# Optimization experiments

Measured on AMD Instinct MI355X. Metric: run time of the kernel, lower is better.

Reference implementation:

```python
import jax, jax.numpy as jnp
import numpy as np

N = 4096
D_MODEL = 512


def setup_inputs() -> dict:
    key = jax.random.key(0)
    ks = jax.random.split(key, 5)
    scale = 1.0 / np.sqrt(D_MODEL)
    return {
        "x": jax.random.normal(ks[0], (N, D_MODEL), dtype=jnp.float32),
        "Wq": jax.random.normal(ks[1], (D_MODEL, D_MODEL), dtype=jnp.float32) * scale,
        "Wk": jax.random.normal(ks[2], (D_MODEL, D_MODEL), dtype=jnp.float32) * scale,
        "Wv": jax.random.normal(ks[3], (D_MODEL, D_MODEL), dtype=jnp.float32) * scale,
        "Ws": jax.random.normal(ks[4], (1, D_MODEL), dtype=jnp.float32) * scale,
    }


def reference(x, Wq, Wk, Wv, Ws):
    # x: [N, d]; torch nn.Linear(bias=False) computes x @ W.T
    Q = x @ Wq.T  # [N, d]
    K = x @ Wk.T  # [N, d]
    V = x @ Wv.T  # [N, d]
    sigma = jnp.clip(x @ Ws.T, 0.001, 1.0)  # [N, 1]

    # prior association: Gaussian kernel over |i - j| with per-row sigma
    pos = jnp.arange(sigma.shape[0], dtype=jnp.float32)
    diff = jnp.abs(pos[:, None] - pos[None, :])  # [N, N]
    gaussian = jnp.exp(-0.5 * (diff / sigma) ** 2) / jnp.sqrt(2.0 * jnp.pi * sigma)
    P = gaussian / (gaussian.sum(axis=1, keepdims=True) + 1e-8)

    scale = jnp.sqrt(jnp.float32(x.shape[-1]))
    S = jax.nn.softmax((Q @ K.T) / scale, axis=-1)  # [N, N]
    Z = S @ V  # [N, d]
    return Z, P, S
```

## Files before the change

kernel.cpp:

```cpp
#include <hip/hip_runtime.h>
#include <math.h>

#define N_TOK 4096
#define DM 512

typedef _Float16 f16x8 __attribute__((ext_vector_type(8)));
typedef _Float16 f16x4 __attribute__((ext_vector_type(4)));
typedef float f32x4 __attribute__((ext_vector_type(4)));

__device__ __forceinline__ void async_ld16(const ushort* g, ushort* l) {
  __builtin_amdgcn_global_load_lds(
      (const __attribute__((address_space(1))) void*)g,
      (__attribute__((address_space(3))) void*)l, 16, 0, 0);
}

template <int N>
__device__ __forceinline__ void vm_wait() {
  asm volatile("s_waitcnt vmcnt(%0)" ::"i"(N) : "memory");
}

__global__ __launch_bounds__(256) void pack_sigma(
    const float* __restrict__ x, const float* __restrict__ Wq,
    const float* __restrict__ Wk, const float* __restrict__ Wv,
    const float* __restrict__ Ws, _Float16* __restrict__ x16,
    _Float16* __restrict__ Wc16, float* __restrict__ sg) {
  const int b = blockIdx.x;
  const int t = threadIdx.x;
  if (b < 2048) {
    int i = b * 1024 + t * 4;
    float4 v = *(const float4*)&x[i];
    f16x4 o;
    o.x = (_Float16)v.x; o.y = (_Float16)v.y;
    o.z = (_Float16)v.z; o.w = (_Float16)v.w;
    *(f16x4*)&x16[i] = o;
    int col = (t * 4) & 511;
    float4 w = *(const float4*)&Ws[col];
    float p = v.x * w.x + v.y * w.y + v.z * w.z + v.w * w.w;
    __shared__ float red[256];
    red[t] = p;
    __syncthreads();
    int lt = t & 127;
    for (int off = 64; off > 0; off >>= 1) {
      if (lt < off) red[t] += red[t + off];
      __syncthreads();
    }
    if (lt == 0) {
      float s = red[t];
      sg[2 * b + (t >> 7)] = fminf(fmaxf(s, 0.001f), 1.0f);
    }
  } else {
    int e = (b - 2048) * 1024 + t * 4;
    const float* src;
    int le = e & (DM * DM - 1);
    if (e < DM * DM) src = Wq + le;
    else if (e < 2 * DM * DM) src = Wk + le;
    else src = Wv + le;
    float4 v = *(const float4*)src;
    f16x4 o;
    o.x = (_Float16)v.x; o.y = (_Float16)v.y;
    o.z = (_Float16)v.z; o.w = (_Float16)v.w;
    *(f16x4*)&Wc16[e] = o;
  }
}

template <int BM, int BN, int BK, int NT, int EPI, int FUSE_P>
__global__ __launch_bounds__(256) void gemm_pipe(
    const _Float16* __restrict__ A, int lda, const _Float16* __restrict__ B,
    int ldb, float scale, float* __restrict__ Cf, _Float16* __restrict__ D0,
    _Float16* __restrict__ D1, _Float16* __restrict__ D2,
    const float* __restrict__ sigma, float* __restrict__ P) {
  constexpr int TB = (BM + BN) * BK;
  constexpr int ACH = BM * BK / 8;
  constexpr int BCH = BN * BK / 8;
  constexpr int L = (ACH + BCH) / 256;
  constexpr int MI = BM / 32;
  constexpr int NJ = BN / 32;
  __shared__ _Float16 lds[3 * TB];
  const int t = threadIdx.x;

  if (FUSE_P && blockIdx.y >= 64) {
    float* red = (float*)lds;
    const int pidx = (blockIdx.y - 64) * 4 + blockIdx.x;
    const int w = t >> 6, lane = t & 63;
#pragma unroll 1
    for (int rr = 0; rr < 4; ++rr) {
      const int i = pidx * 4 + rr;
      const float sgv = sigma[i];
      const float inv2 = -0.5f / (sgv * sgv);
      const float cc = rsqrtf(6.283185307179586f * sgv);
      float4 g[4];
      float sum = 0.f;
#pragma unroll
      for (int r = 0; r < 4; ++r) {
        int j = r * 1024 + t * 4;
        float d0 = (float)(i - j);
        float d1 = d0 - 1.f, d2 = d0 - 2.f, d3 = d0 - 3.f;
        g[r].x = __expf(inv2 * d0 * d0) * cc;
        g[r].y = __expf(inv2 * d1 * d1) * cc;
        g[r].z = __expf(inv2 * d2 * d2) * cc;
        g[r].w = __expf(inv2 * d3 * d3) * cc;
        sum += g[r].x + g[r].y + g[r].z + g[r].w;
      }
#pragma unroll
      for (int off = 32; off > 0; off >>= 1) sum += __shfl_xor(sum, off);
      if (lane == 0) red[w] = sum;
      __syncthreads();
      const float inv = 1.0f / (red[0] + red[1] + red[2] + red[3] + 1e-8f);
      float* Prow = P + (size_t)i * N_TOK;
#pragma unroll
      for (int r = 0; r < 4; ++r) {
        g[r].x *= inv; g[r].y *= inv; g[r].z *= inv; g[r].w *= inv;
        *(float4*)&Prow[r * 1024 + t * 4] = g[r];
      }
      __syncthreads();
    }
    return;
  }

  const int w = t >> 6, Ln = t & 63;
  const int wm = (w >> 1) * (BM / 2), wn = (w & 1) * (BN / 2);
  const int row = Ln & 15, quad = Ln >> 4;
  const int bm = blockIdx.y * BM, bn = blockIdx.x * BN;

  f32x4 acc[MI][NJ] = {{}};

  const ushort* gp[L];
#pragma unroll
  for (int k = 0; k < L; ++k) {
    int c = t + k * 256;
    if (c < ACH) {
      int r = c / (BK / 8), c8 = c % (BK / 8);
      gp[k] = (const ushort*)(A + (size_t)(bm + r) * lda + c8 * 8);
    } else {
      int cb = c - ACH;
      int r = cb / (BK / 8), c8 = cb % (BK / 8);
      gp[k] = (const ushort*)(B + (size_t)(bn + r) * ldb + c8 * 8);
    }
  }

  auto stage = [&](int buf) {
    _Float16* dst = lds + buf * TB;
#pragma unroll
    for (int k = 0; k < L; ++k) {
      async_ld16(gp[k], (ushort*)(dst + (t + k * 256) * 8));
      gp[k] += BK;
    }
  };

  stage(0);
  stage(1);

  for (int tt = 0; tt < NT; ++tt) {
    const int cur = tt % 3;
    if (tt + 2 < NT) stage((tt + 2) % 3);
    if (tt < NT - 2) vm_wait<2 * L>();
    else if (tt == NT - 2) vm_wait<L>();
    else vm_wait<0>();
    __builtin_amdgcn_s_barrier();

    const _Float16* Ah = lds + cur * TB;
    const _Float16* Bh = Ah + BM * BK;
    f16x8 af[BK / 32][MI], bf[BK / 32][NJ];
#pragma unroll
    for (int kk = 0; kk < BK / 32; ++kk) {
#pragma unroll
      for (int i = 0; i < MI; ++i)
        af[kk][i] =
            *(const f16x8*)&Ah[(wm + i * 16 + row) * BK + kk * 32 + quad * 8];
#pragma unroll
      for (int j = 0; j < NJ; ++j)
        bf[kk][j] =
            *(const f16x8*)&Bh[(wn + j * 16 + row) * BK + kk * 32 + quad * 8];
    }
#pragma unroll
    for (int kk = 0; kk < BK / 32; ++kk)
#pragma unroll
      for (int i = 0; i < MI; ++i)
#pragma unroll
        for (int j = 0; j < NJ; ++j)
          acc[i][j] = __builtin_amdgcn_mfma_f32_16x16x32_f16(
              af[kk][i], bf[kk][j], acc[i][j], 0, 0, 0);

    asm volatile("s_waitcnt lgkmcnt(0)" ::: "memory");
    __builtin_amdgcn_s_barrier();
  }

  if constexpr (EPI == 1) {
    const int region = bn >> 9;
    _Float16* D = (region == 0) ? D0 : ((region == 1) ? D1 : D2);
#pragma unroll
    for (int i = 0; i < MI; ++i)
#pragma unroll
      for (int j = 0; j < NJ; ++j)
#pragma unroll
        for (int r = 0; r < 4; ++r) {
          int gr = bm + wm + i * 16 + quad * 4 + r;
          int nn = (bn & 511) + wn + j * 16 + row;
          D[(size_t)gr * 512 + nn] = (_Float16)acc[i][j][r];
        }
  } else if constexpr (EPI == 3) {
#pragma unroll
    for (int i = 0; i < MI; ++i)
#pragma unroll
      for (int j = 0; j < NJ; ++j)
#pragma unroll
        for (int r = 0; r < 4; ++r) {
          int gr = bm + wm + i * 16 + quad * 4 + r;
          int gc = bn + wn + j * 16 + row;
          D0[(size_t)gr * N_TOK + gc] = (_Float16)(acc[i][j][r] * scale);
        }
  } else {
#pragma unroll
    for (int i = 0; i < MI; ++i)
#pragma unroll
      for (int j = 0; j < NJ; ++j)
#pragma unroll
        for (int r = 0; r < 4; ++r) {
          int gr = bm + wm + i * 16 + quad * 4 + r;
          int gc = bn + wn + j * 16 + row;
          Cf[(size_t)gr * DM + gc] = acc[i][j][r];
        }
  }
}

__global__ __launch_bounds__(256) void transpose16(
    const _Float16* __restrict__ V16, _Float16* __restrict__ VT) {
  __shared__ _Float16 T[32][34];
  const int t = threadIdx.x;
  const int r = t >> 3, c4 = (t & 7) * 4;
  f16x4 v = *(const f16x4*)&V16[(size_t)(blockIdx.y * 32 + r) * 512 +
                                blockIdx.x * 32 + c4];
  T[r][c4] = v.x; T[r][c4 + 1] = v.y; T[r][c4 + 2] = v.z; T[r][c4 + 3] = v.w;
  __syncthreads();
  f16x4 o;
  o.x = T[c4][r]; o.y = T[c4 + 1][r]; o.z = T[c4 + 2][r]; o.w = T[c4 + 3][r];
  *(f16x4*)&VT[(size_t)(blockIdx.x * 32 + r) * 4096 + blockIdx.y * 32 + c4] = o;
}

__global__ __launch_bounds__(256) void softmax_kernel(
    _Float16* __restrict__ Sc, float* __restrict__ S) {
  __shared__ float red[256];
  const int t = threadIdx.x;
  _Float16* Srow16 = Sc + (size_t)blockIdx.x * N_TOK;
  float* Srow = S + (size_t)blockIdx.x * N_TOK;
  float f[16];
  float m = -INFINITY;
#pragma unroll
  for (int r = 0; r < 4; ++r) {
    f16x4 h = *(const f16x4*)&Srow16[r * 1024 + t * 4];
    f[r * 4 + 0] = (float)h.x; f[r * 4 + 1] = (float)h.y;
    f[r * 4 + 2] = (float)h.z; f[r * 4 + 3] = (float)h.w;
    m = fmaxf(m, fmaxf(fmaxf(f[r * 4], f[r * 4 + 1]),
                       fmaxf(f[r * 4 + 2], f[r * 4 + 3])));
  }
  red[t] = m;
  __syncthreads();
  for (int off = 128; off > 0; off >>= 1) {
    if (t < off) red[t] = fmaxf(red[t], red[t + off]);
    __syncthreads();
  }
  m = red[0];
  __syncthreads();
  float sum = 0.f;
#pragma unroll
  for (int i = 0; i < 16; ++i) {
    f[i] = __expf(f[i] - m);
    sum += f[i];
  }
  red[t] = sum;
  __syncthreads();
  for (int off = 128; off > 0; off >>= 1) {
    if (t < off) red[t] += red[t + off];
    __syncthreads();
  }
  const float inv = 1.0f / red[0];
#pragma unroll
  for (int r = 0; r < 4; ++r) {
    float4 o;
    o.x = f[r * 4 + 0] * inv; o.y = f[r * 4 + 1] * inv;
    o.z = f[r * 4 + 2] * inv; o.w = f[r * 4 + 3] * inv;
    *(float4*)&Srow[r * 1024 + t * 4] = o;
    f16x4 h;
    h.x = (_Float16)o.x; h.y = (_Float16)o.y;
    h.z = (_Float16)o.z; h.w = (_Float16)o.w;
    *(f16x4*)&Srow16[r * 1024 + t * 4] = h;
  }
}

__global__ __launch_bounds__(256) void tailP(const float* __restrict__ sigma,
                                             float* __restrict__ P) {
  __shared__ float red[256];
  const int t = threadIdx.x;
  const int i = blockIdx.x;
  const float sg = sigma[i];
  const float inv2 = -0.5f / (sg * sg);
  const float c = rsqrtf(6.283185307179586f * sg);
  float4 g[4];
  float sum = 0.f;
#pragma unroll
  for (int r = 0; r < 4; ++r) {
    int j = r * 1024 + t * 4;
    float d0 = (float)(i - j);
    float d1 = d0 - 1.f, d2 = d0 - 2.f, d3 = d0 - 3.f;
    g[r].x = __expf(inv2 * d0 * d0) * c;
    g[r].y = __expf(inv2 * d1 * d1) * c;
    g[r].z = __expf(inv2 * d2 * d2) * c;
    g[r].w = __expf(inv2 * d3 * d3) * c;
    sum += g[r].x + g[r].y + g[r].z + g[r].w;
  }
  red[t] = sum;
  __syncthreads();
  for (int off = 128; off > 0; off >>= 1) {
    if (t < off) red[t] += red[t + off];
    __syncthreads();
  }
  const float inv = 1.0f / (red[0] + 1e-8f);
  float* Prow = P + (size_t)i * N_TOK;
#pragma unroll
  for (int r = 0; r < 4; ++r) {
    g[r].x *= inv; g[r].y *= inv; g[r].z *= inv; g[r].w *= inv;
    *(float4*)&Prow[r * 1024 + t * 4] = g[r];
  }
}

extern "C" void kernel_launch(void* const* d_in, const int* in_sizes, int n_in,
                              void* d_out, int out_size, void* d_ws,
                              size_t ws_size, hipStream_t stream) {
  const float* x = (const float*)d_in[0];
  const float* Wq = (const float*)d_in[1];
  const float* Wk = (const float*)d_in[2];
  const float* Wv = (const float*)d_in[3];
  const float* Ws = (const float*)d_in[4];

  float* out = (float*)d_out;
  float* Z = out;
  float* Pout = Z + (size_t)N_TOK * DM;
  float* S = Pout + (size_t)N_TOK * N_TOK;

  const size_t E = (size_t)N_TOK * DM;

  _Float16* x16 = (_Float16*)d_ws;
  _Float16* Wc16 = x16 + E;
  float* sg = (float*)(Wc16 + 3 * DM * DM);
  _Float16* stage = (_Float16*)(sg + 4096);

  const size_t stage_bytes = (4 * E + (size_t)N_TOK * N_TOK) * sizeof(_Float16);
  const size_t base_bytes = (size_t)((char*)stage - (char*)d_ws);
  const bool ws_ok = ws_size >= base_bytes + stage_bytes;

  _Float16* Q16 = ws_ok ? stage : (_Float16*)Pout;
  _Float16* K16 = Q16 + E;
  _Float16* V16 = K16 + E;
  _Float16* VT16 = V16 + E;
  _Float16* Sc16 = VT16 + E;

  const dim3 blk(256);
  const float qk_scale = 1.0f / sqrtf((float)DM);

  pack_sigma<<<2816, blk, 0, stream>>>(x, Wq, Wk, Wv, Ws, x16, Wc16, sg);

  gemm_pipe<128, 128, 32, 16, 1, 0><<<dim3(12, 32), blk, 0, stream>>>(
      x16, DM, Wc16, DM, 1.0f, nullptr, Q16, K16, V16, nullptr, nullptr);

  transpose16<<<dim3(16, 128), blk, 0, stream>>>(V16, VT16);

  gemm_pipe<256, 128, 32, 16, 3, 0><<<dim3(32, 16), blk, 0, stream>>>(
      Q16, DM, K16, DM, qk_scale, nullptr, Sc16, nullptr, nullptr, nullptr,
      nullptr);

  softmax_kernel<<<N_TOK, blk, 0, stream>>>(Sc16, S);

  if (ws_ok) {
    gemm_pipe<64, 128, 64, 64, 2, 1><<<dim3(4, 64 + 256), blk, 0, stream>>>(
        Sc16, N_TOK, VT16, N_TOK, 1.0f, Z, nullptr, nullptr, nullptr, sg, Pout);
  } else {
    gemm_pipe<64, 128, 64, 64, 2, 0><<<dim3(4, 64), blk, 0, stream>>>(
        Sc16, N_TOK, VT16, N_TOK, 1.0f, Z, nullptr, nullptr, nullptr, nullptr,
        nullptr);
    tailP<<<N_TOK, blk, 0, stream>>>(sg, Pout);
  }
}
```

Before: 244.6 us.

## Fuse softmax into QK epilogue stats and SV GEMM, drop separate transpose kernel

The QK GEMM epilogue now computes per-row partial max and sum-exp over its 128-column tile and writes them to a stats buffer. A new fused kernel merges these stats and runs three kinds of blocks: the SV GEMM normalizes raw scores on the fly when loading A fragments, other blocks write the normalized float S, and the rest compute P. The V projection epilogue writes V transposed through LDS, which removes the transpose kernel. The goal is to cut the separate softmax pass (a read and rewrite of the fp16 score matrix) and two launches, at the cost of extra exp work inside the GEMM inner loop and an extra pass that re-reads raw scores.

```diff
diff --git a/kernel.cpp b/kernel.cpp
--- a/kernel.cpp
+++ b/kernel.cpp
@@ -63,12 +63,12 @@
   }
 }
 
-template <int BM, int BN, int BK, int NT, int EPI, int FUSE_P>
+template <int BM, int BN, int BK, int NT, int EPI>
 __global__ __launch_bounds__(256) void gemm_pipe(
     const _Float16* __restrict__ A, int lda, const _Float16* __restrict__ B,
-    int ldb, float scale, float* __restrict__ Cf, _Float16* __restrict__ D0,
+    int ldb, float scale, _Float16* __restrict__ D0,
     _Float16* __restrict__ D1, _Float16* __restrict__ D2,
-    const float* __restrict__ sigma, float* __restrict__ P) {
+    float2* __restrict__ Part) {
   constexpr int TB = (BM + BN) * BK;
   constexpr int ACH = BM * BK / 8;
   constexpr int BCH = BN * BK / 8;
@@ -78,10 +78,170 @@
   __shared__ _Float16 lds[3 * TB];
   const int t = threadIdx.x;
 
-  if (FUSE_P && blockIdx.y >= 64) {
+  const int w = t >> 6, Ln = t & 63;
+  const int wm = (w >> 1) * (BM / 2), wn = (w & 1) * (BN / 2);
+  const int row = Ln & 15, quad = Ln >> 4;
+  const int bm = blockIdx.y * BM, bn = blockIdx.x * BN;
+
+  f32x4 acc[MI][NJ] = {{}};
+
+  const ushort* gp[L];
+#pragma unroll
+  for (int k = 0; k < L; ++k) {
+    int c = t + k * 256;
+    if (c < ACH) {
+      int r = c / (BK / 8), c8 = c % (BK / 8);
+      gp[k] = (const ushort*)(A + (size_t)(bm + r) * lda + c8 * 8);
+    } else {
+      int cb = c - ACH;
+      int r = cb / (BK / 8), c8 = cb % (BK / 8);
+      gp[k] = (const ushort*)(B + (size_t)(bn + r) * ldb + c8 * 8);
+    }
+  }
+
+  auto stage = [&](int buf) {
+    _Float16* dst = lds + buf * TB;
+#pragma unroll
+    for (int k = 0; k < L; ++k) {
+      async_ld16(gp[k], (ushort*)(dst + (t + k * 256) * 8));
+      gp[k] += BK;
+    }
+  };
+
+  stage(0);
+  stage(1);
+
+  for (int tt = 0; tt < NT; ++tt) {
+    const int cur = tt % 3;
+    if (tt + 2 < NT) stage((tt + 2) % 3);
+    if (tt < NT - 2) vm_wait<2 * L>();
+    else if (tt == NT - 2) vm_wait<L>();
+    else vm_wait<0>();
+    __builtin_amdgcn_s_barrier();
+
+    const _Float16* Ah = lds + cur * TB;
+    const _Float16* Bh = Ah + BM * BK;
+    f16x8 af[BK / 32][MI], bf[BK / 32][NJ];
+#pragma unroll
+    for (int kk = 0; kk < BK / 32; ++kk) {
+#pragma unroll
+      for (int i = 0; i < MI; ++i)
+        af[kk][i] =
+            *(const f16x8*)&Ah[(wm + i * 16 + row) * BK + kk * 32 + quad * 8];
+#pragma unroll
+      for (int j = 0; j < NJ; ++j)
+        bf[kk][j] =
+            *(const f16x8*)&Bh[(wn + j * 16 + row) * BK + kk * 32 + quad * 8];
+    }
+#pragma unroll
+    for (int kk = 0; kk < BK / 32; ++kk)
+#pragma unroll
+      for (int i = 0; i < MI; ++i)
+#pragma unroll
+        for (int j = 0; j < NJ; ++j)
+          acc[i][j] = __builtin_amdgcn_mfma_f32_16x16x32_f16(
+              af[kk][i], bf[kk][j], acc[i][j], 0, 0, 0);
+
+    asm volatile("s_waitcnt lgkmcnt(0)" ::: "memory");
+    __builtin_amdgcn_s_barrier();
+  }
+
+  if constexpr (EPI == 1) {
+    const int region = bn >> 9;
+    if (region < 2) {
+      _Float16* D = (region == 0) ? D0 : D1;
+#pragma unroll
+      for (int i = 0; i < MI; ++i)
+#pragma unroll
+        for (int j = 0; j < NJ; ++j)
+#pragma unroll
+          for (int r = 0; r < 4; ++r) {
+            int gr = bm + wm + i * 16 + quad * 4 + r;
+            int nn = (bn & 511) + wn + j * 16 + row;
+            D[(size_t)gr * 512 + nn] = (_Float16)acc[i][j][r];
+          }
+    } else {
+      _Float16* T = lds;
+#pragma unroll
+      for (int i = 0; i < MI; ++i)
+#pragma unroll
+        for (int j = 0; j < NJ; ++j) {
+          int nn = wn + j * 16 + row;
+          int gr0 = wm + i * 16 + quad * 4;
+          f16x4 v;
+          v.x = (_Float16)acc[i][j][0]; v.y = (_Float16)acc[i][j][1];
+          v.z = (_Float16)acc[i][j][2]; v.w = (_Float16)acc[i][j][3];
+          *(f16x4*)&T[nn * 136 + gr0] = v;
+        }
+      __syncthreads();
+#pragma unroll
+      for (int c = 0; c < 8; ++c) {
+        int cc = t + c * 256;
+        int nn = cc >> 4;
+        int g8 = (cc & 15) * 8;
+        f16x8 v = *(const f16x8*)&T[nn * 136 + g8];
+        *(f16x8*)&D2[(size_t)((bn & 511) + nn) * 4096 + bm + g8] = v;
+      }
+    }
+  } else {
+    float2* Ml = (float2*)lds;
+#pragma unroll
+    for (int i = 0; i < MI; ++i)
+#pragma unroll
+      for (int r = 0; r < 4; ++r) {
+        float sv[NJ];
+        int gr = bm + wm + i * 16 + quad * 4 + r;
+#pragma unroll
+        for (int j = 0; j < NJ; ++j) {
+          _Float16 h = (_Float16)(acc[i][j][r] * scale);
+          D0[(size_t)gr * N_TOK + bn + wn + j * 16 + row] = h;
+          sv[j] = (float)h;
+        }
+        float m = sv[0];
+#pragma unroll
+        for (int j = 1; j < NJ; ++j) m = fmaxf(m, sv[j]);
+#pragma unroll
+        for (int off = 1; off < 16; off <<= 1)
+          m = fmaxf(m, __shfl_xor(m, off));
+        float se = 0.f;
+#pragma unroll
+        for (int j = 0; j < NJ; ++j) se += __expf(sv[j] - m);
+#pragma unroll
+        for (int off = 1; off < 16; off <<= 1) se += __shfl_xor(se, off);
+        if (row == 0) {
+          int rb = wm + i * 16 + quad * 4 + r;
+          Ml[(w & 1) * BM + rb] = make_float2(m, se);
+        }
+      }
+    __syncthreads();
+    {
+      float2 a = Ml[t];
+      float2 b2 = Ml[BM + t];
+      float m = fmaxf(a.x, b2.x);
+      float l = a.y * __expf(a.x - m) + b2.y * __expf(b2.x - m);
+      Part[(size_t)(bm + t) * 32 + blockIdx.x] = make_float2(m, l);
+    }
+  }
+}
+
+template <int WITH_P>
+__global__ __launch_bounds__(256) void sv_fused(
+    const _Float16* __restrict__ Sc, const float2* __restrict__ stats,
+    const _Float16* __restrict__ VT, float* __restrict__ Z,
+    float* __restrict__ S, const float* __restrict__ sigma,
+    float* __restrict__ P) {
+  constexpr int BM = 64, BN = 128, BK = 64, NT = N_TOK / BK;
+  constexpr int TB = (BM + BN) * BK;
+  constexpr int ACH = BM * BK / 8;
+  constexpr int L = (ACH + BN * BK / 8) / 256;
+  __shared__ _Float16 lds[3 * TB];
+  const int t = threadIdx.x;
+  const int b = blockIdx.x;
+
+  if (WITH_P && b >= 512) {
     float* red = (float*)lds;
-    const int pidx = (blockIdx.y - 64) * 4 + blockIdx.x;
-    const int w = t >> 6, lane = t & 63;
+    const int pidx = b - 512;
+    const int wv = t >> 6, lane = t & 63;
 #pragma unroll 1
     for (int rr = 0; rr < 4; ++rr) {
       const int i = pidx * 4 + rr;
@@ -103,7 +263,7 @@
       }
 #pragma unroll
       for (int off = 32; off > 0; off >>= 1) sum += __shfl_xor(sum, off);
-      if (lane == 0) red[w] = sum;
+      if (lane == 0) red[wv] = sum;
       __syncthreads();
       const float inv = 1.0f / (red[0] + red[1] + red[2] + red[3] + 1e-8f);
       float* Prow = P + (size_t)i * N_TOK;
@@ -117,27 +277,102 @@
     return;
   }
 
+  if (b >= 256) {
+    const int rs = (b - 256) * 16;
+    float2* pm = (float2*)lds;
+    float* sm = (float*)(pm + 256);
+    float* si = sm + 16;
+    {
+      int rr = t >> 4, kh = t & 15;
+      float2 p0 = stats[(size_t)(rs + rr) * 32 + 2 * kh];
+      float2 p1 = stats[(size_t)(rs + rr) * 32 + 2 * kh + 1];
+      float m = fmaxf(p0.x, p1.x);
+      float l = p0.y * __expf(p0.x - m) + p1.y * __expf(p1.x - m);
+      pm[t] = make_float2(m, l);
+    }
+    __syncthreads();
+    if (t < 16) {
+      float m = -INFINITY, l = 0.f;
+#pragma unroll
+      for (int k = 0; k < 16; ++k) {
+        float2 pr = pm[t * 16 + k];
+        float nm = fmaxf(m, pr.x);
+        l = l * __expf(m - nm) + pr.y * __expf(pr.x - nm);
+        m = nm;
+      }
+      sm[t] = m;
+      si[t] = 1.0f / l;
+    }
+    __syncthreads();
+#pragma unroll 1
+    for (int r = 0; r < 16; ++r) {
+      const int rowg = rs + r;
+      const float m = sm[r], linv = si[r];
+      const _Float16* src = Sc + (size_t)rowg * N_TOK + t * 16;
+      float* dst = S + (size_t)rowg * N_TOK + t * 16;
+      f16x8 h0 = *(const f16x8*)src;
+      f16x8 h1 = *(const f16x8*)(src + 8);
+      float4 o0, o1, o2, o3;
+      o0.x = __expf((float)h0[0] - m) * linv;
+      o0.y = __expf((float)h0[1] - m) * linv;
+      o0.z = __expf((float)h0[2] - m) * linv;
+      o0.w = __expf((float)h0[3] - m) * linv;
+      o1.x = __expf((float)h0[4] - m) * linv;
+      o1.y = __expf((float)h0[5] - m) * linv;
+      o1.z = __expf((float)h0[6] - m) * linv;
+      o1.w = __expf((float)h0[7] - m) * linv;
+      o2.x = __expf((float)h1[0] - m) * linv;
+      o2.y = __expf((float)h1[1] - m) * linv;
+      o2.z = __expf((float)h1[2] - m) * linv;
+      o2.w = __expf((float)h1[3] - m) * linv;
+      o3.x = __expf((float)h1[4] - m) * linv;
+      o3.y = __expf((float)h1[5] - m) * linv;
+      o3.z = __expf((float)h1[6] - m) * linv;
+      o3.w = __expf((float)h1[7] - m) * linv;
+      *(float4*)(dst + 0) = o0;
+      *(float4*)(dst + 4) = o1;
+      *(float4*)(dst + 8) = o2;
+      *(float4*)(dst + 12) = o3;
+    }
+    return;
+  }
+
   const int w = t >> 6, Ln = t & 63;
-  const int wm = (w >> 1) * (BM / 2), wn = (w & 1) * (BN / 2);
+  const int wm = (w >> 1) * 32, wn = (w & 1) * 64;
   const int row = Ln & 15, quad = Ln >> 4;
-  const int bm = blockIdx.y * BM, bn = blockIdx.x * BN;
-
-  f32x4 acc[MI][NJ] = {{}};
+  const int bm = (b >> 2) * BM, bn = (b & 3) * BN;
+
+  float mrow[2], linv[2];
+#pragma unroll
+  for (int i = 0; i < 2; ++i) {
+    const int gr = bm + wm + i * 16 + row;
+    float m = -INFINITY, l = 0.f;
+#pragma unroll
+    for (int kb = 0; kb < 32; ++kb) {
+      float2 pr = stats[(size_t)gr * 32 + kb];
+      float nm = fmaxf(m, pr.x);
+      l = l * __expf(m - nm) + pr.y * __expf(pr.x - nm);
+      m = nm;
+    }
+    mrow[i] = m;
+    linv[i] = 1.0f / l;
+  }
+
+  f32x4 acc[2][4] = {{}};
 
   const ushort* gp[L];
 #pragma unroll
   for (int k = 0; k < L; ++k) {
     int c = t + k * 256;
     if (c < ACH) {
-      int r = c / (BK / 8), c8 = c % (BK / 8);
-      gp[k] = (const ushort*)(A + (size_t)(bm + r) * lda + c8 * 8);
+      int r = c >> 3, c8 = c & 7;
+      gp[k] = (const ushort*)(Sc + (size_t)(bm + r) * N_TOK + c8 * 8);
     } else {
       int cb = c - ACH;
-      int r = cb / (BK / 8), c8 = cb % (BK / 8);
-      gp[k] = (const ushort*)(B + (size_t)(bn + r) * ldb + c8 * 8);
-    }
-  }
-
+      int r = cb >> 3, c8 = cb & 7;
+      gp[k] = (const ushort*)(VT + (size_t)(bn + r) * N_TOK + c8 * 8);
+    }
+  }
   auto stage = [&](int buf) {
     _Float16* dst = lds + buf * TB;
 #pragma unroll
@@ -160,24 +395,30 @@
 
     const _Float16* Ah = lds + cur * TB;
     const _Float16* Bh = Ah + BM * BK;
-    f16x8 af[BK / 32][MI], bf[BK / 32][NJ];
-#pragma unroll
-    for (int kk = 0; kk < BK / 32; ++kk) {
-#pragma unroll
-      for (int i = 0; i < MI; ++i)
-        af[kk][i] =
-            *(const f16x8*)&Ah[(wm + i * 16 + row) * BK + kk * 32 + quad * 8];
-#pragma unroll
-      for (int j = 0; j < NJ; ++j)
+    f16x8 af[2][2], bf[2][4];
+#pragma unroll
+    for (int kk = 0; kk < 2; ++kk) {
+#pragma unroll
+      for (int i = 0; i < 2; ++i) {
+        f16x8 raw = *(const f16x8*)&Ah[(wm + i * 16 + row) * BK + kk * 32 +
+                                       quad * 8];
+        f16x8 pa;
+#pragma unroll
+        for (int e = 0; e < 8; ++e)
+          pa[e] = (_Float16)(__expf((float)raw[e] - mrow[i]) * linv[i]);
+        af[kk][i] = pa;
+      }
+#pragma unroll
+      for (int j = 0; j < 4; ++j)
         bf[kk][j] =
             *(const f16x8*)&Bh[(wn + j * 16 + row) * BK + kk * 32 + quad * 8];
     }
 #pragma unroll
-    for (int kk = 0; kk < BK / 32; ++kk)
-#pragma unroll
-      for (int i = 0; i < MI; ++i)
-#pragma unroll
-        for (int j = 0; j < NJ; ++j)
+    for (int kk = 0; kk < 2; ++kk)
+#pragma unroll
+      for (int i = 0; i < 2; ++i)
+#pragma unroll
+        for (int j = 0; j < 4; ++j)
           acc[i][j] = __builtin_amdgcn_mfma_f32_16x16x32_f16(
               af[kk][i], bf[kk][j], acc[i][j], 0, 0, 0);
 
@@ -185,106 +426,16 @@
     __builtin_amdgcn_s_barrier();
   }
 
-  if constexpr (EPI == 1) {
-    const int region = bn >> 9;
-    _Float16* D = (region == 0) ? D0 : ((region == 1) ? D1 : D2);
-#pragma unroll
-    for (int i = 0; i < MI; ++i)
-#pragma unroll
-      for (int j = 0; j < NJ; ++j)
-#pragma unroll
-        for (int r = 0; r < 4; ++r) {
-          int gr = bm + wm + i * 16 + quad * 4 + r;
-          int nn = (bn & 511) + wn + j * 16 + row;
-          D[(size_t)gr * 512 + nn] = (_Float16)acc[i][j][r];
-        }
-  } else if constexpr (EPI == 3) {
-#pragma unroll
-    for (int i = 0; i < MI; ++i)
-#pragma unroll
-      for (int j = 0; j < NJ; ++j)
-#pragma unroll
-        for (int r = 0; r < 4; ++r) {
-          int gr = bm + wm + i * 16 + quad * 4 + r;
-          int gc = bn + wn + j * 16 + row;
-          D0[(size_t)gr * N_TOK + gc] = (_Float16)(acc[i][j][r] * scale);
-        }
-  } else {
-#pragma unroll
-    for (int i = 0; i < MI; ++i)
-#pragma unroll
-      for (int j = 0; j < NJ; ++j)
-#pragma unroll
-        for (int r = 0; r < 4; ++r) {
-          int gr = bm + wm + i * 16 + quad * 4 + r;
-          int gc = bn + wn + j * 16 + row;
-          Cf[(size_t)gr * DM + gc] = acc[i][j][r];
-        }
-  }
-}
-
-__global__ __launch_bounds__(256) void transpose16(
-    const _Float16* __restrict__ V16, _Float16* __restrict__ VT) {
-  __shared__ _Float16 T[32][34];
-  const int t = threadIdx.x;
-  const int r = t >> 3, c4 = (t & 7) * 4;
-  f16x4 v = *(const f16x4*)&V16[(size_t)(blockIdx.y * 32 + r) * 512 +
-                                blockIdx.x * 32 + c4];
-  T[r][c4] = v.x; T[r][c4 + 1] = v.y; T[r][c4 + 2] = v.z; T[r][c4 + 3] = v.w;
-  __syncthreads();
-  f16x4 o;
-  o.x = T[c4][r]; o.y = T[c4 + 1][r]; o.z = T[c4 + 2][r]; o.w = T[c4 + 3][r];
-  *(f16x4*)&VT[(size_t)(blockIdx.x * 32 + r) * 4096 + blockIdx.y * 32 + c4] = o;
-}
-
-__global__ __launch_bounds__(256) void softmax_kernel(
-    _Float16* __restrict__ Sc, float* __restrict__ S) {
-  __shared__ float red[256];
-  const int t = threadIdx.x;
-  _Float16* Srow16 = Sc + (size_t)blockIdx.x * N_TOK;
-  float* Srow = S + (size_t)blockIdx.x * N_TOK;
-  float f[16];
-  float m = -INFINITY;
-#pragma unroll
-  for (int r = 0; r < 4; ++r) {
-    f16x4 h = *(const f16x4*)&Srow16[r * 1024 + t * 4];
-    f[r * 4 + 0] = (float)h.x; f[r * 4 + 1] = (float)h.y;
-    f[r * 4 + 2] = (float)h.z; f[r * 4 + 3] = (float)h.w;
-    m = fmaxf(m, fmaxf(fmaxf(f[r * 4], f[r * 4 + 1]),
-                       fmaxf(f[r * 4 + 2], f[r * 4 + 3])));
-  }
-  red[t] = m;
-  __syncthreads();
-  for (int off = 128; off > 0; off >>= 1) {
-    if (t < off) red[t] = fmaxf(red[t], red[t + off]);
-    __syncthreads();
-  }
-  m = red[0];
-  __syncthreads();
-  float sum = 0.f;
-#pragma unroll
-  for (int i = 0; i < 16; ++i) {
-    f[i] = __expf(f[i] - m);
-    sum += f[i];
-  }
-  red[t] = sum;
-  __syncthreads();
-  for (int off = 128; off > 0; off >>= 1) {
-    if (t < off) red[t] += red[t + off];
-    __syncthreads();
-  }
-  const float inv = 1.0f / red[0];
-#pragma unroll
-  for (int r = 0; r < 4; ++r) {
-    float4 o;
-    o.x = f[r * 4 + 0] * inv; o.y = f[r * 4 + 1] * inv;
-    o.z = f[r * 4 + 2] * inv; o.w = f[r * 4 + 3] * inv;
-    *(float4*)&Srow[r * 1024 + t * 4] = o;
-    f16x4 h;
-    h.x = (_Float16)o.x; h.y = (_Float16)o.y;
-    h.z = (_Float16)o.z; h.w = (_Float16)o.w;
-    *(f16x4*)&Srow16[r * 1024 + t * 4] = h;
-  }
+#pragma unroll
+  for (int i = 0; i < 2; ++i)
+#pragma unroll
+    for (int j = 0; j < 4; ++j)
+#pragma unroll
+      for (int r = 0; r < 4; ++r) {
+        int gr = bm + wm + i * 16 + quad * 4 + r;
+        int gc = bn + wn + j * 16 + row;
+        Z[(size_t)gr * DM + gc] = acc[i][j][r];
+      }
 }
 
 __global__ __launch_bounds__(256) void tailP(const float* __restrict__ sigma,
@@ -342,16 +493,16 @@
   _Float16* x16 = (_Float16*)d_ws;
   _Float16* Wc16 = x16 + E;
   float* sg = (float*)(Wc16 + 3 * DM * DM);
-  _Float16* stage = (_Float16*)(sg + 4096);
-
-  const size_t stage_bytes = (4 * E + (size_t)N_TOK * N_TOK) * sizeof(_Float16);
+  float2* pstats = (float2*)(sg + 4096);
+  _Float16* stage = (_Float16*)(pstats + (size_t)N_TOK * 32);
+
+  const size_t stage_bytes = (3 * E + (size_t)N_TOK * N_TOK) * sizeof(_Float16);
   const size_t base_bytes = (size_t)((char*)stage - (char*)d_ws);
   const bool ws_ok = ws_size >= base_bytes + stage_bytes;
 
   _Float16* Q16 = ws_ok ? stage : (_Float16*)Pout;
   _Float16* K16 = Q16 + E;
-  _Float16* V16 = K16 + E;
-  _Float16* VT16 = V16 + E;
+  _Float16* VT16 = K16 + E;
   _Float16* Sc16 = VT16 + E;
 
   const dim3 blk(256);
@@ -359,24 +510,18 @@
 
   pack_sigma<<<2816, blk, 0, stream>>>(x, Wq, Wk, Wv, Ws, x16, Wc16, sg);
 
-  gemm_pipe<128, 128, 32, 16, 1, 0><<<dim3(12, 32), blk, 0, stream>>>(
-      x16, DM, Wc16, DM, 1.0f, nullptr, Q16, K16, V16, nullptr, nullptr);
-
-  transpose16<<<dim3(16, 128), blk, 0, stream>>>(V16, VT16);
-
-  gemm_pipe<256, 128, 32, 16, 3, 0><<<dim3(32, 16), blk, 0, stream>>>(
-      Q16, DM, K16, DM, qk_scale, nullptr, Sc16, nullptr, nullptr, nullptr,
-      nullptr);
-
-  softmax_kernel<<<N_TOK, blk, 0, stream>>>(Sc16, S);
+  gemm_pipe<128, 128, 32, 16, 1><<<dim3(12, 32), blk, 0, stream>>>(
+      x16, DM, Wc16, DM, 1.0f, Q16, K16, VT16, nullptr);
+
+  gemm_pipe<256, 128, 32, 16, 3><<<dim3(32, 16), blk, 0, stream>>>(
+      Q16, DM, K16, DM, qk_scale, Sc16, nullptr, nullptr, pstats);
 
   if (ws_ok) {
-    gemm_pipe<64, 128, 64, 64, 2, 1><<<dim3(4, 64 + 256), blk, 0, stream>>>(
-        Sc16, N_TOK, VT16, N_TOK, 1.0f, Z, nullptr, nullptr, nullptr, sg, Pout);
+    sv_fused<1><<<dim3(1536), blk, 0, stream>>>(Sc16, pstats, VT16, Z, S, sg,
+                                                Pout);
   } else {
-    gemm_pipe<64, 128, 64, 64, 2, 0><<<dim3(4, 64), blk, 0, stream>>>(
-        Sc16, N_TOK, VT16, N_TOK, 1.0f, Z, nullptr, nullptr, nullptr, nullptr,
-        nullptr);
+    sv_fused<0><<<dim3(512), blk, 0, stream>>>(Sc16, pstats, VT16, Z, S,
+                                               nullptr, nullptr);
     tailP<<<N_TOK, blk, 0, stream>>>(sg, Pout);
   }
 }
```

New measurement: 274.9 us. 1.12x slower.
